# Optimization experiments

Measured on AMD Instinct MI355X. Metric: run time of the kernel, lower is better.

## Reference

```python
import jax, jax.numpy as jnp
import numpy as np
from jax import lax

B, H, W, CIN, COUT, K, SDIM = 8, 256, 256, 128, 128, 3, 512


def setup_inputs() -> dict:
    key = jax.random.key(0)
    k1, k2, k3, k4, k5 = jax.random.split(key, 5)
    return {
        "x": jax.random.normal(k1, (B, H, W, CIN), dtype=jnp.float32),
        "style": jax.random.normal(k2, (B, SDIM), dtype=jnp.float32),
        "kernel": jax.random.normal(k3, (K, K, CIN, COUT), dtype=jnp.float32),
        "w_mod": jax.random.normal(k4, (SDIM, CIN), dtype=jnp.float32) / np.sqrt(SDIM),
        "b_mod": jnp.zeros((CIN,), dtype=jnp.float32),
        "noise_strength": jnp.zeros((1,), dtype=jnp.float32),
        "bias": jnp.zeros((COUT,), dtype=jnp.float32),
        "noise": jax.random.normal(k5, (B, H, W, 1), dtype=jnp.float32),
    }


def reference(x, style, kernel, w_mod, b_mod, noise_strength, bias, noise):
    kh, kw, cin, cout = kernel.shape
    # equalized-lr runtime coefficient
    he_std = 1.0 / jnp.sqrt(jnp.asarray(kh * kw * cin, jnp.float32))
    w = kernel * he_std  # [kh,kw,cin,cout]
    # style modulation (Dense with zero constant bias) + 1
    s = style @ w_mod + b_mod + 1.0  # [B, cin]
    # demodulate=True: normalize by global max-abs of style (as in source)
    s = s * (1.0 / jnp.max(jnp.abs(s)))
    # NOTE: source uses style[0] only -> single shared modulated weight
    w = w * s[0][None, None, :, None]
    d = lax.rsqrt(jnp.sum(jnp.square(w), axis=(0, 1, 2)) + 1e-8)  # [cout]
    w = w * d[None, None, None, :]
    # plain conv branch: NHWC, stride 1, SAME padding
    y = lax.conv_general_dilated(
        x, w, window_strides=(1, 1), padding="SAME",
        dimension_numbers=("NHWC", "HWIO", "NHWC"))
    # noise injection (noise_strength is zero-init, kept for faithfulness)
    y = y + noise * (noise_strength / 2.0)
    y = y + bias
    # lrelu(0.2) * sqrt(2)
    y = jnp.where(y >= 0, y, 0.2 * y) * jnp.sqrt(jnp.asarray(2.0, y.dtype))
    return y
```

## Files before the change

kernel.cpp:

```cpp
#include <hip/hip_runtime.h>
#include <hip/hip_bf16.h>

#define H 256
#define W 256
#define CIN 128
#define COUT 128
#define BATCH 8
#define LDA 136

typedef float f32x4 __attribute__((ext_vector_type(4)));
typedef short bf16x8 __attribute__((ext_vector_type(8)));

static __device__ __forceinline__ unsigned short f2bf(float f) {
    unsigned int x = __float_as_uint(f);
    unsigned int r = (x + 0x7fffu + ((x >> 16) & 1u)) >> 16;
    return (unsigned short)r;
}

__global__ __launch_bounds__(1024) void prep_kernel(
    const float* __restrict__ style, const float* __restrict__ kern,
    const float* __restrict__ w_mod, const float* __restrict__ b_mod,
    unsigned short* __restrict__ wprep)
{
    __shared__ float sbuf[1024];
    __shared__ float scaleArr[CIN];
    __shared__ float dArr[COUT];
    const int t = threadIdx.x;
    const int b = t >> 7;
    const int c = t & 127;

    float acc = 0.f;
    const float4* st4 = (const float4*)(style + b * 512);
    for (int k4 = 0; k4 < 128; ++k4) {
        float4 s4 = st4[k4];
        int k = k4 * 4;
        acc += s4.x * w_mod[(k + 0) * CIN + c];
        acc += s4.y * w_mod[(k + 1) * CIN + c];
        acc += s4.z * w_mod[(k + 2) * CIN + c];
        acc += s4.w * w_mod[(k + 3) * CIN + c];
    }
    float sval = acc + b_mod[c] + 1.0f;

    sbuf[t] = fabsf(sval);
    __syncthreads();
    for (int off = 512; off > 0; off >>= 1) {
        if (t < off) sbuf[t] = fmaxf(sbuf[t], sbuf[t + off]);
        __syncthreads();
    }
    float invmax = 1.0f / sbuf[0];
    const float he_std = 1.0f / sqrtf(1152.0f);
    if (t < CIN) scaleArr[t] = sval * invmax * he_std;
    __syncthreads();

    {
        const int co = t & 127;
        const int slice = t >> 7;
        float ss = 0.f;
        for (int j = 0; j < 144; ++j) {
            int i = slice * 144 + j;
            int ci = i & 127;
            float wv = kern[i * 128 + co] * scaleArr[ci];
            ss += wv * wv;
        }
        sbuf[t] = ss;
        __syncthreads();
        if (t < 128) {
            float sum = 0.f;
            for (int sl = 0; sl < 8; ++sl) sum += sbuf[sl * 128 + t];
            dArr[t] = rsqrtf(sum + 1e-8f);
        }
        __syncthreads();
    }

    for (int u = t; u < 9 * 4 * 8 * 64; u += 1024) {
        int lane  = u & 63;
        int ntile = (u >> 6) & 7;
        int kc    = (u >> 9) & 3;
        int kk    = u >> 11;
        int co  = ntile * 16 + (lane & 15);
        int cib = kc * 32 + (lane >> 4) * 8;
        float dv = dArr[co];
        unsigned int packed[4];
        for (int jp = 0; jp < 4; ++jp) {
            int ci0 = cib + jp * 2;
            float w0 = kern[(kk * 128 + ci0)     * 128 + co] * scaleArr[ci0]     * dv;
            float w1 = kern[(kk * 128 + ci0 + 1) * 128 + co] * scaleArr[ci0 + 1] * dv;
            packed[jp] = (unsigned int)f2bf(w0) | ((unsigned int)f2bf(w1) << 16);
        }
        ((uint4*)wprep)[u] = make_uint4(packed[0], packed[1], packed[2], packed[3]);
    }
}

__global__ __launch_bounds__(256) void conv_kernel(
    const float* __restrict__ x, const unsigned short* __restrict__ wprep,
    const float* __restrict__ noise_strength, const float* __restrict__ bias,
    const float* __restrict__ noise, float* __restrict__ out)
{
    __shared__ unsigned short ldsA[130 * LDA];
    const int tid  = threadIdx.x;
    const int lane = tid & 63;
    const int wave = tid >> 6;
    const int wm = wave & 1;
    const int wn = wave >> 1;
    const int wt = blockIdx.x;
    const int h  = blockIdx.y;
    const int b  = blockIdx.z;
    const int wstart = wt * 128;

    f32x4 acc[4][4];
    const f32x4 zero = {0.f, 0.f, 0.f, 0.f};
    for (int i = 0; i < 4; ++i)
        for (int j = 0; j < 4; ++j) acc[i][j] = zero;

    for (int kh = 0; kh < 3; ++kh) {
        __syncthreads();
        const int hImg = h + kh - 1;
        const bool rowValid = (hImg >= 0) && (hImg < H);
        const float* rowPtr = x + ((size_t)(b * H + hImg) * W) * CIN;
        for (int idx = tid; idx < 130 * 32; idx += 256) {
            int p  = idx >> 5;
            int c4 = idx & 31;
            int wImg = wstart - 1 + p;
            float4 v = make_float4(0.f, 0.f, 0.f, 0.f);
            if (rowValid && (unsigned)wImg < (unsigned)W)
                v = *(const float4*)(rowPtr + (size_t)wImg * CIN + c4 * 4);
            ushort4 u;
            u.x = f2bf(v.x); u.y = f2bf(v.y); u.z = f2bf(v.z); u.w = f2bf(v.w);
            *(ushort4*)&ldsA[p * LDA + c4 * 4] = u;
        }
        __syncthreads();

        #pragma unroll
        for (int kw = 0; kw < 3; ++kw) {
            const int kk = kh * 3 + kw;
            #pragma unroll
            for (int kc = 0; kc < 4; ++kc) {
                bf16x8 bfrag[4], afrag[4];
                const bf16x8* bptr = (const bf16x8*)wprep +
                                     (((kk * 4 + kc) * 8 + wn * 4) * 64 + lane);
                #pragma unroll
                for (int j = 0; j < 4; ++j) bfrag[j] = bptr[j * 64];
                const int ka = kc * 32 + (lane >> 4) * 8;
                #pragma unroll
                for (int i = 0; i < 4; ++i) {
                    int m = wm * 64 + i * 16 + (lane & 15) + kw;
                    afrag[i] = *(const bf16x8*)&ldsA[m * LDA + ka];
                }
                #pragma unroll
                for (int i = 0; i < 4; ++i)
                    #pragma unroll
                    for (int j = 0; j < 4; ++j)
                        acc[i][j] = __builtin_amdgcn_mfma_f32_16x16x32_bf16(
                            afrag[i], bfrag[j], acc[i][j], 0, 0, 0);
            }
        }
    }

    const float ns  = noise_strength[0] * 0.5f;
    const float RT2 = 1.41421356237309515f;
    const size_t pixBase = ((size_t)(b * H + h) * W) + wstart;
    #pragma unroll
    for (int i = 0; i < 4; ++i) {
        const int mbase = wm * 64 + i * 16 + ((lane >> 4) << 2);
        #pragma unroll
        for (int r = 0; r < 4; ++r) {
            const size_t pix = pixBase + (mbase + r);
            const float nz = noise[pix] * ns;
            #pragma unroll
            for (int j = 0; j < 4; ++j) {
                const int col = wn * 64 + j * 16 + (lane & 15);
                float v = acc[i][j][r] + nz + bias[col];
                v = (v >= 0.f ? v : 0.2f * v) * RT2;
                out[pix * COUT + col] = v;
            }
        }
    }
}

extern "C" void kernel_launch(void* const* d_in, const int* in_sizes, int n_in,
                              void* d_out, int out_size, void* d_ws, size_t ws_size,
                              hipStream_t stream) {
    const float* x              = (const float*)d_in[0];
    const float* style          = (const float*)d_in[1];
    const float* kern           = (const float*)d_in[2];
    const float* w_mod          = (const float*)d_in[3];
    const float* b_mod          = (const float*)d_in[4];
    const float* noise_strength = (const float*)d_in[5];
    const float* bias           = (const float*)d_in[6];
    const float* noise          = (const float*)d_in[7];
    float* out = (float*)d_out;
    unsigned short* wprep = (unsigned short*)d_ws;

    hipLaunchKernelGGL(prep_kernel, dim3(1), dim3(1024), 0, stream,
                       style, kern, w_mod, b_mod, wprep);
    hipLaunchKernelGGL(conv_kernel, dim3(2, 256, 8), dim3(256), 0, stream,
                       x, wprep, noise_strength, bias, noise, out);
}
```

Baseline: 741.9 us.

## Split single-block weight prep into three multi-block kernels

The single-block prep kernel, which did style modulation, demodulation and weight swizzling on one workgroup, is split into three kernels: a per-batch style modulation with max reduction (8 blocks), per-tap partial sums of squares (9 blocks), and a swizzle/pack kernel (72 blocks). Intermediate values pass through device globals. This spreads the serial prep work across many CUs and adds two extra kernel launches and global round trips. The prep stage is small next to the conv kernel, so any effect on total time is likely small.

```diff
diff --git a/kernel.cpp b/kernel.cpp
--- a/kernel.cpp
+++ b/kernel.cpp
@@ -17,78 +17,114 @@
     return (unsigned short)r;
 }
 
-__global__ __launch_bounds__(1024) void prep_kernel(
-    const float* __restrict__ style, const float* __restrict__ kern,
-    const float* __restrict__ w_mod, const float* __restrict__ b_mod,
-    unsigned short* __restrict__ wprep)
-{
-    __shared__ float sbuf[1024];
-    __shared__ float scaleArr[CIN];
+__device__ float g_s0[CIN];
+__device__ float g_bmax[BATCH];
+__device__ float g_partial[9 * COUT];
+
+__global__ __launch_bounds__(256) void mod_style(
+    const float* __restrict__ style, const float* __restrict__ w_mod,
+    const float* __restrict__ b_mod)
+{
+    __shared__ float red[256];
+    const int t = threadIdx.x;
+    const int b = blockIdx.x;
+    const int c = t & 127;
+    const int half = t >> 7;
+
+    float acc = 0.f;
+    const float4* st4 = (const float4*)(style + b * 512 + half * 256);
+    const float* wm = w_mod + half * 256 * CIN + c;
+    for (int k4 = 0; k4 < 64; ++k4) {
+        float4 s4 = st4[k4];
+        const float* w = wm + k4 * 4 * CIN;
+        acc += s4.x * w[0 * CIN];
+        acc += s4.y * w[1 * CIN];
+        acc += s4.z * w[2 * CIN];
+        acc += s4.w * w[3 * CIN];
+    }
+    red[t] = acc;
+    __syncthreads();
+    if (t < 128) {
+        float sval = red[t] + red[t + 128] + b_mod[t] + 1.0f;
+        if (b == 0) g_s0[t] = sval;
+        red[t] = fabsf(sval);
+    }
+    __syncthreads();
+    for (int off = 64; off > 0; off >>= 1) {
+        if (t < off) red[t] = fmaxf(red[t], red[t + off]);
+        __syncthreads();
+    }
+    if (t == 0) g_bmax[b] = red[0];
+}
+
+__global__ __launch_bounds__(256) void demod_partial(
+    const float* __restrict__ kern)
+{
+    __shared__ float scale[CIN];
+    __shared__ float red[256];
+    const int t = threadIdx.x;
+    const int kk = blockIdx.x;
+    const int co = t & 127;
+    const int half = t >> 7;
+
+    if (t < 128) {
+        float m = g_bmax[0];
+        #pragma unroll
+        for (int i = 1; i < BATCH; ++i) m = fmaxf(m, g_bmax[i]);
+        const float he_std = 1.0f / sqrtf(1152.0f);
+        scale[t] = g_s0[t] * (1.0f / m) * he_std;
+    }
+    __syncthreads();
+
+    float ss = 0.f;
+    const float* kbase = kern + (size_t)kk * 128 * 128 + co;
+    for (int j = 0; j < 64; ++j) {
+        int ci = half * 64 + j;
+        float wv = kbase[(size_t)ci * 128] * scale[ci];
+        ss += wv * wv;
+    }
+    red[t] = ss;
+    __syncthreads();
+    if (t < 128) g_partial[kk * 128 + t] = red[t] + red[t + 128];
+}
+
+__global__ __launch_bounds__(256) void swizzle_kernel(
+    const float* __restrict__ kern, unsigned short* __restrict__ wprep)
+{
+    __shared__ float scale[CIN];
     __shared__ float dArr[COUT];
     const int t = threadIdx.x;
-    const int b = t >> 7;
-    const int c = t & 127;
-
-    float acc = 0.f;
-    const float4* st4 = (const float4*)(style + b * 512);
-    for (int k4 = 0; k4 < 128; ++k4) {
-        float4 s4 = st4[k4];
-        int k = k4 * 4;
-        acc += s4.x * w_mod[(k + 0) * CIN + c];
-        acc += s4.y * w_mod[(k + 1) * CIN + c];
-        acc += s4.z * w_mod[(k + 2) * CIN + c];
-        acc += s4.w * w_mod[(k + 3) * CIN + c];
-    }
-    float sval = acc + b_mod[c] + 1.0f;
-
-    sbuf[t] = fabsf(sval);
-    __syncthreads();
-    for (int off = 512; off > 0; off >>= 1) {
-        if (t < off) sbuf[t] = fmaxf(sbuf[t], sbuf[t + off]);
-        __syncthreads();
-    }
-    float invmax = 1.0f / sbuf[0];
-    const float he_std = 1.0f / sqrtf(1152.0f);
-    if (t < CIN) scaleArr[t] = sval * invmax * he_std;
-    __syncthreads();
-
-    {
-        const int co = t & 127;
-        const int slice = t >> 7;
-        float ss = 0.f;
-        for (int j = 0; j < 144; ++j) {
-            int i = slice * 144 + j;
-            int ci = i & 127;
-            float wv = kern[i * 128 + co] * scaleArr[ci];
-            ss += wv * wv;
-        }
-        sbuf[t] = ss;
-        __syncthreads();
-        if (t < 128) {
-            float sum = 0.f;
-            for (int sl = 0; sl < 8; ++sl) sum += sbuf[sl * 128 + t];
-            dArr[t] = rsqrtf(sum + 1e-8f);
-        }
-        __syncthreads();
-    }
-
-    for (int u = t; u < 9 * 4 * 8 * 64; u += 1024) {
-        int lane  = u & 63;
-        int ntile = (u >> 6) & 7;
-        int kc    = (u >> 9) & 3;
-        int kk    = u >> 11;
-        int co  = ntile * 16 + (lane & 15);
-        int cib = kc * 32 + (lane >> 4) * 8;
-        float dv = dArr[co];
-        unsigned int packed[4];
-        for (int jp = 0; jp < 4; ++jp) {
-            int ci0 = cib + jp * 2;
-            float w0 = kern[(kk * 128 + ci0)     * 128 + co] * scaleArr[ci0]     * dv;
-            float w1 = kern[(kk * 128 + ci0 + 1) * 128 + co] * scaleArr[ci0 + 1] * dv;
-            packed[jp] = (unsigned int)f2bf(w0) | ((unsigned int)f2bf(w1) << 16);
-        }
-        ((uint4*)wprep)[u] = make_uint4(packed[0], packed[1], packed[2], packed[3]);
-    }
+    const int u = blockIdx.x * 256 + t;
+
+    if (t < 128) {
+        float m = g_bmax[0];
+        #pragma unroll
+        for (int i = 1; i < BATCH; ++i) m = fmaxf(m, g_bmax[i]);
+        const float he_std = 1.0f / sqrtf(1152.0f);
+        scale[t] = g_s0[t] * (1.0f / m) * he_std;
+        float sum = 0.f;
+        #pragma unroll
+        for (int g = 0; g < 9; ++g) sum += g_partial[g * 128 + t];
+        dArr[t] = rsqrtf(sum + 1e-8f);
+    }
+    __syncthreads();
+
+    const int lane  = u & 63;
+    const int ntile = (u >> 6) & 7;
+    const int kc    = (u >> 9) & 3;
+    const int kk    = u >> 11;
+    const int co  = ntile * 16 + (lane & 15);
+    const int cib = kc * 32 + (lane >> 4) * 8;
+    const float dv = dArr[co];
+    unsigned int packed[4];
+    #pragma unroll
+    for (int jp = 0; jp < 4; ++jp) {
+        int ci0 = cib + jp * 2;
+        float w0 = kern[(kk * 128 + ci0)     * 128 + co] * scale[ci0]     * dv;
+        float w1 = kern[(kk * 128 + ci0 + 1) * 128 + co] * scale[ci0 + 1] * dv;
+        packed[jp] = (unsigned int)f2bf(w0) | ((unsigned int)f2bf(w1) << 16);
+    }
+    ((uint4*)wprep)[u] = make_uint4(packed[0], packed[1], packed[2], packed[3]);
 }
 
 __global__ __launch_bounds__(256) void conv_kernel(
@@ -191,8 +227,11 @@
     float* out = (float*)d_out;
     unsigned short* wprep = (unsigned short*)d_ws;
 
-    hipLaunchKernelGGL(prep_kernel, dim3(1), dim3(1024), 0, stream,
-                       style, kern, w_mod, b_mod, wprep);
+    hipLaunchKernelGGL(mod_style, dim3(8), dim3(256), 0, stream,
+                       style, w_mod, b_mod);
+    hipLaunchKernelGGL(demod_partial, dim3(9), dim3(256), 0, stream, kern);
+    hipLaunchKernelGGL(swizzle_kernel, dim3(72), dim3(256), 0, stream,
+                       kern, wprep);
     hipLaunchKernelGGL(conv_kernel, dim3(2, 256, 8), dim3(256), 0, stream,
                        x, wprep, noise_strength, bias, noise, out);
 }
```

After: 700.2 us. 1.06x faster.
